# Kernel tuning notes

Measured on AMD Instinct MI355X. Metric: run time of the kernel, lower is better.

The kernel has to match this reference:

```python
import jax, jax.numpy as jnp
import numpy as np
from jax import lax

CAP_UNITS = 49
CAP_SIZE = 8

def setup_inputs() -> dict:
    key = jax.random.key(0)
    k1, k2, k3 = jax.random.split(key, 3)
    x = jax.random.normal(k1, (128, 16, 64, 64), dtype=jnp.float32)
    # 49 ConvUnits (16->8, 9x9) stacked into one conv weight [49*8, 16, 9, 9]
    fan_in = 16 * 9 * 9
    bound = 1.0 / np.sqrt(fan_in)
    W = jax.random.uniform(k2, (CAP_UNITS * CAP_SIZE, 16, 9, 9), jnp.float32, -bound, bound)
    b = jax.random.uniform(k3, (CAP_UNITS * CAP_SIZE,), jnp.float32, -bound, bound)
    return {"x": x, "W": W, "b": b}

def squash(s, axis):
    mag_sq = jnp.sum(s * s, axis=axis, keepdims=True)
    mag = jnp.sqrt(mag_sq)
    return mag_sq / (1.0 + mag_sq) * (s / mag)

def reference(x, W, b):
    B = x.shape[0]
    # single fused conv == 49 parallel 16->8 convs, 9x9, stride 2, VALID
    h = lax.conv_general_dilated(
        x, W, window_strides=(2, 2), padding='VALID',
        dimension_numbers=('NCHW', 'OIHW', 'NCHW'))
    h = h + b[None, :, None, None]                    # [B, 49*8, H', W']
    Hp, Wp = h.shape[2], h.shape[3]
    u = h.reshape(B, CAP_UNITS, CAP_SIZE, Hp * Wp)    # [B, 49, 8, HW]
    # torch ordering: cat over units on dim 3 -> [B,8,HW,49] -> flatten -> capsule idx = hw*49 + unit
    u = u.transpose(0, 3, 1, 2).reshape(B, Hp * Wp * CAP_UNITS, CAP_SIZE)
    return squash(u, axis=2)
```

## Files before the change

kernel.cpp:

```cpp
#include <hip/hip_runtime.h>


typedef __attribute__((ext_vector_type(8)))  short short8;
typedef __attribute__((ext_vector_type(16))) float f32x16;

constexpr int Bn = 128, Units = 49, Cap = 8, OW = 28, HWp = 784;
constexpr int Nn = 392, Npad = 448;
constexpr int BM = 256, BNt = 64, NB = 7;
constexpr int NSLOT = 82;
constexpr size_t XW_BYTES = (size_t)Bn * 64 * 64 * 16 * 2;
constexpr size_t BW_BYTES = (size_t)NSLOT * 2 * Npad * 8 * 2;

__device__ inline unsigned short f2bf(float f) {
    unsigned u = __float_as_uint(f);
    u += 0x7FFF + ((u >> 16) & 1);
    return (unsigned short)(u >> 16);
}

__global__ __launch_bounds__(256) void prep_x(const float* __restrict__ x,
                                              unsigned short* __restrict__ xw) {
    __shared__ unsigned short tile[64 * 16];
    const int b = blockIdx.x >> 6, y = blockIdx.x & 63;
    const int t = threadIdx.x;
    const int c = t >> 4, x0 = (t & 15) * 4;
    const float4 v = *(const float4*)(x + (((size_t)b * 16 + c) * 64 + y) * 64 + x0);
    tile[(x0 + 0) * 16 + c] = f2bf(v.x);
    tile[(x0 + 1) * 16 + c] = f2bf(v.y);
    tile[(x0 + 2) * 16 + c] = f2bf(v.z);
    tile[(x0 + 3) * 16 + c] = f2bf(v.w);
    __syncthreads();
    const ushort4 o = *(const ushort4*)&tile[t * 4];
    *(ushort4*)(xw + (size_t)blockIdx.x * 1024 + t * 4) = o;
}

__global__ __launch_bounds__(256) void prep_w(const float* __restrict__ W,
                                              unsigned short* __restrict__ bw) {
    const int idx = blockIdx.x * 256 + threadIdx.x;
    if (idx >= NSLOT * 2 * Npad) return;
    const int n  = idx % Npad;
    const int ph = idx / Npad;
    const int h = ph & 1, p = ph >> 1;
    unsigned short vals[8];
    if (p < 81 && n < Nn) {
#pragma unroll
        for (int j = 0; j < 8; ++j)
            vals[j] = f2bf(W[(size_t)(n * 16 + h * 8 + j) * 81 + p]);
    } else {
#pragma unroll
        for (int j = 0; j < 8; ++j) vals[j] = 0;
    }
    *(ushort4*)(bw + (size_t)idx * 8)     = make_ushort4(vals[0], vals[1], vals[2], vals[3]);
    *(ushort4*)(bw + (size_t)idx * 8 + 4) = make_ushort4(vals[4], vals[5], vals[6], vals[7]);
}

#define MFMA32(A, B, C) __builtin_amdgcn_mfma_f32_32x32x16_bf16(A, B, C, 0, 0, 0)

__global__ __launch_bounds__(256, 2) void pcaps_mfma32(
    const unsigned short* __restrict__ xw,
    const unsigned short* __restrict__ bw,
    const float* __restrict__ bias,
    float* __restrict__ out)
{
    __shared__ int tbl[84];
    const int t = threadIdx.x;
    if (t < 84) tbl[t] = (t < 81) ? (t / 9) * 2048 + (t % 9) * 32 : 0;

    const int cpx  = gridDim.x >> 3;
    const int wgid = (blockIdx.x & 7) * cpx + (blockIdx.x >> 3);
    const int nb = wgid % NB, mb = wgid / NB;
    const int n0 = nb * BNt;

    const int w = t >> 6, l = t & 63;
    const int r = l & 31, h = l >> 5;

    int abase[2];
#pragma unroll
    for (int mi = 0; mi < 2; ++mi) {
        const int m = mb * BM + w * 64 + mi * 32 + r;
        const int b = m / HWp;
        const int hw = m - b * HWp;
        const int oy = hw / OW, ox = hw - oy * OW;
        abase[mi] = b * 131072 + oy * 4096 + ox * 64 + h * 16;
    }
    const int bb0 = ((h * Npad) + n0 + r) * 16;

    f32x16 acc[2][2];
#pragma unroll
    for (int mi = 0; mi < 2; ++mi)
#pragma unroll
        for (int ni = 0; ni < 2; ++ni)
#pragma unroll
            for (int e = 0; e < 16; ++e) acc[mi][ni][e] = 0.f;

    __syncthreads();

    const char* __restrict__ xc = (const char*)xw;
    const char* __restrict__ bc = (const char*)bw;

    int kA = tbl[0], kB = tbl[1];
    short8 aA0 = *(const short8*)(xc + (abase[0] + kA));
    short8 aA1 = *(const short8*)(xc + (abase[1] + kA));
    short8 bA0 = *(const short8*)(bc + bb0);
    short8 bA1 = *(const short8*)(bc + (bb0 + 512));
    short8 aB0 = *(const short8*)(xc + (abase[0] + kB));
    short8 aB1 = *(const short8*)(xc + (abase[1] + kB));
    short8 bB0 = *(const short8*)(bc + (bb0 + 14336));
    short8 bB1 = *(const short8*)(bc + (bb0 + 14336 + 512));
    int bbA = bb0 + 2 * 14336;
    int bbB = bb0 + 3 * 14336;

    for (int s = 0; s < 40; ++s) {
        const int k2 = tbl[2 * s + 2], k3 = tbl[2 * s + 3];

        acc[0][0] = MFMA32(aA0, bA0, acc[0][0]);
        acc[0][1] = MFMA32(aA0, bA1, acc[0][1]);
        acc[1][0] = MFMA32(aA1, bA0, acc[1][0]);
        acc[1][1] = MFMA32(aA1, bA1, acc[1][1]);
        aA0 = *(const short8*)(xc + (abase[0] + k2));
        aA1 = *(const short8*)(xc + (abase[1] + k2));
        bA0 = *(const short8*)(bc + bbA);
        bA1 = *(const short8*)(bc + (bbA + 512));
        bbA += 28672;

        acc[0][0] = MFMA32(aB0, bB0, acc[0][0]);
        acc[0][1] = MFMA32(aB0, bB1, acc[0][1]);
        acc[1][0] = MFMA32(aB1, bB0, acc[1][0]);
        acc[1][1] = MFMA32(aB1, bB1, acc[1][1]);
        aB0 = *(const short8*)(xc + (abase[0] + k3));
        aB1 = *(const short8*)(xc + (abase[1] + k3));
        bB0 = *(const short8*)(bc + bbB);
        bB1 = *(const short8*)(bc + (bbB + 512));
        bbB += 28672;
    }
    acc[0][0] = MFMA32(aA0, bA0, acc[0][0]);
    acc[0][1] = MFMA32(aA0, bA1, acc[0][1]);
    acc[1][0] = MFMA32(aA1, bA0, acc[1][0]);
    acc[1][1] = MFMA32(aA1, bA1, acc[1][1]);
    acc[0][0] = MFMA32(aB0, bB0, acc[0][0]);
    acc[0][1] = MFMA32(aB0, bB1, acc[0][1]);
    acc[1][0] = MFMA32(aB1, bB0, acc[1][0]);
    acc[1][1] = MFMA32(aB1, bB1, acc[1][1]);

    float bv[2];
#pragma unroll
    for (int ni = 0; ni < 2; ++ni) {
        const int n = n0 + ni * 32 + r;
        bv[ni] = (n < Nn) ? bias[n] : 0.f;
    }
#pragma unroll
    for (int mi = 0; mi < 2; ++mi) {
#pragma unroll
        for (int ni = 0; ni < 2; ++ni) {
            const int n = n0 + ni * 32 + r;
            const bool nok = (n < Nn);
#pragma unroll
            for (int reg = 0; reg < 16; ++reg) {
                float e = acc[mi][ni][reg] + bv[ni];
                float sq = e * e;
                sq += __shfl_xor(sq, 1);
                sq += __shfl_xor(sq, 2);
                sq += __shfl_xor(sq, 4);
                const float scale = sqrtf(sq) / (1.0f + sq);
                if (nok) {
                    const int rowc = (reg & 3) + 8 * (reg >> 2) + 4 * h;
                    const int m = mb * BM + w * 64 + mi * 32 + rowc;
                    out[(size_t)m * Nn + n] = e * scale;
                }
            }
        }
    }
}

__global__ __launch_bounds__(128) void pcaps_direct(
    const float* __restrict__ x, const float* __restrict__ W,
    const float* __restrict__ bias, float* __restrict__ out)
{
    const int blk = blockIdx.x;
    const int tile = blk % 7;
    const int u = (blk / 7) % Units;
    const int b = blk / (7 * Units);
    const int hw = tile * 128 + threadIdx.x;
    const bool active = (hw < HWp);
    const int oy = active ? (hw / OW) : 0;
    const int ox = active ? (hw % OW) : 0;
    const float* xb = x + (size_t)b * (16 * 64 * 64) + (size_t)(oy * 2) * 64 + ox * 2;
    const float* wu = W + (size_t)u * (Cap * 1296);
    float acc[Cap];
#pragma unroll
    for (int j = 0; j < Cap; ++j) acc[j] = bias[u * Cap + j];
    for (int c = 0; c < 16; ++c) {
        const float* xcp = xb + c * (64 * 64);
        const float* wc = wu + c * 81;
#pragma unroll
        for (int ky = 0; ky < 9; ++ky) {
            const float* xr = xcp + ky * 64;
            float xv[9];
#pragma unroll
            for (int kx = 0; kx < 9; ++kx) xv[kx] = xr[kx];
#pragma unroll
            for (int kx = 0; kx < 9; ++kx)
#pragma unroll
                for (int j = 0; j < Cap; ++j)
                    acc[j] = fmaf(xv[kx], wc[j * 1296 + ky * 9 + kx], acc[j]);
        }
    }
    if (active) {
        float msq = 0.f;
#pragma unroll
        for (int j = 0; j < Cap; ++j) msq = fmaf(acc[j], acc[j], msq);
        const float scale = sqrtf(msq) / (1.0f + msq);
        float* op = out + (size_t)b * (HWp * Nn) + (size_t)hw * Nn + u * Cap;
        float4 o0, o1;
        o0.x = acc[0] * scale; o0.y = acc[1] * scale; o0.z = acc[2] * scale; o0.w = acc[3] * scale;
        o1.x = acc[4] * scale; o1.y = acc[5] * scale; o1.z = acc[6] * scale; o1.w = acc[7] * scale;
        *reinterpret_cast<float4*>(op) = o0;
        *reinterpret_cast<float4*>(op + 4) = o1;
    }
}

extern "C" void kernel_launch(void* const* d_in, const int* in_sizes, int n_in,
                              void* d_out, int out_size, void* d_ws, size_t ws_size,
                              hipStream_t stream)
{
    const float* x  = (const float*)d_in[0];
    const float* W  = (const float*)d_in[1];
    const float* bs = (const float*)d_in[2];
    float* out      = (float*)d_out;

    if (ws_size < XW_BYTES + BW_BYTES) {
        pcaps_direct<<<Bn * Units * 7, 128, 0, stream>>>(x, W, bs, out);
        return;
    }

    unsigned short* xw = (unsigned short*)d_ws;
    unsigned short* bw = (unsigned short*)((char*)d_ws + XW_BYTES);

    prep_x<<<Bn * 64, 256, 0, stream>>>(x, xw);
    prep_w<<<(NSLOT * 2 * Npad + 255) / 256, 256, 0, stream>>>(W, bw);
    pcaps_mfma32<<<(100352 / BM) * NB, 256, 0, stream>>>(xw, bw, bs, out);
}
```

Before: 253.5 us.

## Swap MFMA operands so each lane holds capsule dims, vectorizing squash epilogue

Swaps the A/B operands of the MFMA so the accumulator layout puts output channels (capsule components) along registers rather than lanes. The squash reduction then needs one cross-lane shuffle instead of three per element, and outputs are written as float4 stores along contiguous channels instead of scattered scalar stores. Launch bounds are raised to allow three blocks per CU, which adds register pressure risk.

```diff
diff --git a/kernel.cpp b/kernel.cpp
--- a/kernel.cpp
+++ b/kernel.cpp
@@ -55,7 +55,7 @@
 
 #define MFMA32(A, B, C) __builtin_amdgcn_mfma_f32_32x32x16_bf16(A, B, C, 0, 0, 0)
 
-__global__ __launch_bounds__(256, 2) void pcaps_mfma32(
+__global__ __launch_bounds__(256, 3) void pcaps_mfma32(
     const unsigned short* __restrict__ xw,
     const unsigned short* __restrict__ bw,
     const float* __restrict__ bias,
@@ -86,11 +86,11 @@
 
     f32x16 acc[2][2];
 #pragma unroll
-    for (int mi = 0; mi < 2; ++mi)
-#pragma unroll
-        for (int ni = 0; ni < 2; ++ni)
-#pragma unroll
-            for (int e = 0; e < 16; ++e) acc[mi][ni][e] = 0.f;
+    for (int ni = 0; ni < 2; ++ni)
+#pragma unroll
+        for (int mi = 0; mi < 2; ++mi)
+#pragma unroll
+            for (int e = 0; e < 16; ++e) acc[ni][mi][e] = 0.f;
 
     __syncthreads();
 
@@ -112,59 +112,61 @@
     for (int s = 0; s < 40; ++s) {
         const int k2 = tbl[2 * s + 2], k3 = tbl[2 * s + 3];
 
-        acc[0][0] = MFMA32(aA0, bA0, acc[0][0]);
-        acc[0][1] = MFMA32(aA0, bA1, acc[0][1]);
-        acc[1][0] = MFMA32(aA1, bA0, acc[1][0]);
-        acc[1][1] = MFMA32(aA1, bA1, acc[1][1]);
+        acc[0][0] = MFMA32(bA0, aA0, acc[0][0]);
+        acc[0][1] = MFMA32(bA0, aA1, acc[0][1]);
+        acc[1][0] = MFMA32(bA1, aA0, acc[1][0]);
+        acc[1][1] = MFMA32(bA1, aA1, acc[1][1]);
         aA0 = *(const short8*)(xc + (abase[0] + k2));
         aA1 = *(const short8*)(xc + (abase[1] + k2));
         bA0 = *(const short8*)(bc + bbA);
         bA1 = *(const short8*)(bc + (bbA + 512));
         bbA += 28672;
 
-        acc[0][0] = MFMA32(aB0, bB0, acc[0][0]);
-        acc[0][1] = MFMA32(aB0, bB1, acc[0][1]);
-        acc[1][0] = MFMA32(aB1, bB0, acc[1][0]);
-        acc[1][1] = MFMA32(aB1, bB1, acc[1][1]);
+        acc[0][0] = MFMA32(bB0, aB0, acc[0][0]);
+        acc[0][1] = MFMA32(bB0, aB1, acc[0][1]);
+        acc[1][0] = MFMA32(bB1, aB0, acc[1][0]);
+        acc[1][1] = MFMA32(bB1, aB1, acc[1][1]);
         aB0 = *(const short8*)(xc + (abase[0] + k3));
         aB1 = *(const short8*)(xc + (abase[1] + k3));
         bB0 = *(const short8*)(bc + bbB);
         bB1 = *(const short8*)(bc + (bbB + 512));
         bbB += 28672;
     }
-    acc[0][0] = MFMA32(aA0, bA0, acc[0][0]);
-    acc[0][1] = MFMA32(aA0, bA1, acc[0][1]);
-    acc[1][0] = MFMA32(aA1, bA0, acc[1][0]);
-    acc[1][1] = MFMA32(aA1, bA1, acc[1][1]);
-    acc[0][0] = MFMA32(aB0, bB0, acc[0][0]);
-    acc[0][1] = MFMA32(aB0, bB1, acc[0][1]);
-    acc[1][0] = MFMA32(aB1, bB0, acc[1][0]);
-    acc[1][1] = MFMA32(aB1, bB1, acc[1][1]);
-
-    float bv[2];
-#pragma unroll
-    for (int ni = 0; ni < 2; ++ni) {
-        const int n = n0 + ni * 32 + r;
-        bv[ni] = (n < Nn) ? bias[n] : 0.f;
-    }
+    acc[0][0] = MFMA32(bA0, aA0, acc[0][0]);
+    acc[0][1] = MFMA32(bA0, aA1, acc[0][1]);
+    acc[1][0] = MFMA32(bA1, aA0, acc[1][0]);
+    acc[1][1] = MFMA32(bA1, aA1, acc[1][1]);
+    acc[0][0] = MFMA32(bB0, aB0, acc[0][0]);
+    acc[0][1] = MFMA32(bB0, aB1, acc[0][1]);
+    acc[1][0] = MFMA32(bB1, aB0, acc[1][0]);
+    acc[1][1] = MFMA32(bB1, aB1, acc[1][1]);
+
 #pragma unroll
     for (int mi = 0; mi < 2; ++mi) {
+        const int m = mb * BM + w * 64 + mi * 32 + r;
+        float* __restrict__ orow = out + (size_t)m * Nn;
 #pragma unroll
         for (int ni = 0; ni < 2; ++ni) {
-            const int n = n0 + ni * 32 + r;
-            const bool nok = (n < Nn);
-#pragma unroll
-            for (int reg = 0; reg < 16; ++reg) {
-                float e = acc[mi][ni][reg] + bv[ni];
-                float sq = e * e;
-                sq += __shfl_xor(sq, 1);
-                sq += __shfl_xor(sq, 2);
-                sq += __shfl_xor(sq, 4);
-                const float scale = sqrtf(sq) / (1.0f + sq);
-                if (nok) {
-                    const int rowc = (reg & 3) + 8 * (reg >> 2) + 4 * h;
-                    const int m = mb * BM + w * 64 + mi * 32 + rowc;
-                    out[(size_t)m * Nn + n] = e * scale;
+#pragma unroll
+            for (int q = 0; q < 4; ++q) {
+                const int nqb = n0 + ni * 32 + 8 * q + 4 * h;
+                const bool ok = (nqb < Nn);
+                const float4 bq = *(const float4*)(bias + (ok ? nqb : 0));
+                float e0 = acc[ni][mi][4 * q + 0] + bq.x;
+                float e1 = acc[ni][mi][4 * q + 1] + bq.y;
+                float e2 = acc[ni][mi][4 * q + 2] + bq.z;
+                float e3 = acc[ni][mi][4 * q + 3] + bq.w;
+                float msq = e0 * e0;
+                msq = fmaf(e1, e1, msq);
+                msq = fmaf(e2, e2, msq);
+                msq = fmaf(e3, e3, msq);
+                msq += __shfl_xor(msq, 32);
+                const float scale = sqrtf(msq) / (1.0f + msq);
+                if (ok) {
+                    float4 o;
+                    o.x = e0 * scale; o.y = e1 * scale;
+                    o.z = e2 * scale; o.w = e3 * scale;
+                    *reinterpret_cast<float4*>(orow + nqb) = o;
                 }
             }
         }
```

Result: slower. 445.6 us (+75.8%).
